# Kernel tuning notes

Measured on AMD Instinct MI355X. Metric: run time of the kernel, lower is better.

The kernel has to match this reference:

```python
import jax, jax.numpy as jnp
import numpy as np
from jax import lax

NEG = jnp.float32(-1e30)  # log-domain 'zero'
BLANK = 0


def setup_inputs() -> dict:
    T, N, C, S = 512, 512, 80, 128
    k0, k1, k2, k3 = jax.random.split(jax.random.key(0), 4)
    logits = jax.random.normal(k0, (T, N, C), dtype=jnp.float32)
    log_probs = jax.nn.log_softmax(logits, axis=-1)  # CTCLoss expects log-probs
    targets = jax.random.randint(k1, (N, S), 1, C).astype(jnp.int32)  # labels in [1, C-1], blank=0 excluded
    input_lengths = jax.random.randint(k2, (N,), T // 2, T + 1).astype(jnp.int32)
    target_lengths = jax.random.randint(k3, (N,), S // 2, S + 1).astype(jnp.int32)
    return {"log_probs": log_probs, "targets": targets,
            "input_lengths": input_lengths, "target_lengths": target_lengths}


def _ctc_loss(log_probs, targets, input_lengths, target_lengths):
    # log_probs: (T, N, C) log-probabilities; targets: (N, S) labels (no blanks)
    T, N, C = log_probs.shape
    S = targets.shape[1]
    L = 2 * S + 1  # extended label length: blank-interleaved

    # extended targets: [blank, y1, blank, y2, ..., yS, blank]  -> (N, L)
    ext = jnp.zeros((N, L), jnp.int32).at[:, 1::2].set(targets)
    # skip transition (s-2 -> s) allowed only if ext[s] != ext[s-2]
    # (blank positions have ext[s]==ext[s-2]==blank, so this also forbids blank skips)
    skip_ok = jnp.pad(ext[:, 2:] != ext[:, :-2], ((0, 0), (2, 0)), constant_values=False)

    # emission log-probs on the lattice: (T, N, L)
    emit = jnp.take_along_axis(log_probs, jnp.broadcast_to(ext[None], (T, N, L)), axis=2)

    # alpha at t=0: only lattice positions 0 (blank) and 1 (first label) reachable
    alpha0 = jnp.full((N, L), NEG).at[:, 0].set(emit[0, :, 0]).at[:, 1].set(emit[0, :, 1])

    def step(alpha, xs):
        em, t = xs  # em: (N, L)
        a1 = jnp.pad(alpha[:, :-1], ((0, 0), (1, 0)), constant_values=NEG)
        a2 = jnp.where(skip_ok,
                       jnp.pad(alpha[:, :-2], ((0, 0), (2, 0)), constant_values=NEG), NEG)
        m = jnp.maximum(alpha, jnp.maximum(a1, a2))
        lse = m + jnp.log(jnp.exp(alpha - m) + jnp.exp(a1 - m) + jnp.exp(a2 - m))
        new = lse + em
        # freeze alpha for finished sequences (t >= input_length)
        alpha_new = jnp.where((t < input_lengths)[:, None], new, alpha)
        return alpha_new, None

    alpha_T, _ = lax.scan(step, alpha0, (emit[1:], jnp.arange(1, T, dtype=jnp.int32)))

    # final states: last blank (2*tl) and last label (2*tl - 1)
    i1 = (2 * target_lengths)[:, None]
    v1 = jnp.take_along_axis(alpha_T, i1, axis=1)[:, 0]
    v2 = jnp.take_along_axis(alpha_T, i1 - 1, axis=1)[:, 0]
    m = jnp.maximum(v1, v2)
    loss = -(m + jnp.log(jnp.exp(v1 - m) + jnp.exp(v2 - m)))
    # zero_infinity=True: infeasible alignments -> 0 loss
    loss = jnp.where(jnp.isfinite(loss) & (loss < 1e10), loss, 0.0)
    return loss  # (N,) reduction='none'


def reference(log_probs, targets, input_lengths, target_lengths):
    return _ctc_loss(log_probs, targets, input_lengths, target_lengths)
```

## Files before the change

kernel.cpp:

```cpp
#include <hip/hip_runtime.h>


#define NEGC  (-1.0e30f)
#define LOG2E 1.4426950408889634f
#define LN2   0.6931471805599453f

constexpr int T_ = 512;
constexpr int C_ = 80;
constexpr int S_ = 128;
constexpr int U_ = 8;
constexpr int WROW = 520;

__device__ __forceinline__ float exp2a(float x) { return __builtin_amdgcn_exp2f(x); }
__device__ __forceinline__ float log2a(float x) { return __builtin_amdgcn_logf(x); }

template <int CTRL>
__device__ __forceinline__ float dppf(float old_, float src) {
    return __int_as_float(__builtin_amdgcn_update_dpp(
        __float_as_int(old_), __float_as_int(src), CTRL, 0xF, 0xF, false));
}

__device__ __forceinline__ float lse2(float x, float y) {
    float m = fmaxf(x, y);
    return m + log2a(1.0f + exp2a(-fabsf(x - y)));
}
__device__ __forceinline__ float lse3(float x, float y, float z) {
    float m = fmaxf(x, fmaxf(y, z));
    return m + log2a(exp2a(x - m) + exp2a(y - m) + exp2a(z - m));
}

__global__ __launch_bounds__(64) void ctc_half(
    const float* __restrict__ lp, const int* __restrict__ tgt,
    const int* __restrict__ ilen, const int* __restrict__ tlen,
    float* __restrict__ ws, int N)
{
    const int b   = blockIdx.x;
    const int n   = b >> 1;
    const int dir = b & 1;
    const int l   = threadIdx.x;

    float* ga = ws + (size_t)n * WROW;
    float* gg = ga + 260;

    const int* tn = tgt + n * S_;
    const int ext1 = tn[2 * l];
    const int ext3 = tn[2 * l + 1];
    const int prev = (l > 0) ? tn[2 * l - 1] : 0;
    const bool skip1 = (l > 0) && (ext1 != prev);
    const bool skip3 = (ext3 != ext1);
    const bool skb3  = (l < 63) && (tn[2 * l + 2] != ext3);

    int len = ilen[n];
    len = len < 1 ? 1 : (len > T_ ? T_ : len);
    const int mid = len >> 1;

    const size_t rstride = (size_t)N * C_;
    const float* lpn = lp + (size_t)n * C_;
    const float* pB = lpn;
    const float* p1 = lpn + ext1;
    const float* p3 = lpn + ext3;

    float rb[U_], r1[U_], r3[U_];

    if (dir == 0) {
        const int last = mid - 1 > 0 ? mid - 1 : 0;
        #pragma unroll
        for (int u = 0; u < U_; ++u) {
            const int r = u + 1;
            const int rc = r < mid ? r : last;
            const size_t o = (size_t)rc * rstride;
            rb[r & 7] = pB[o]; r1[r & 7] = p1[o]; r3[r & 7] = p3[o];
        }
        float a0 = NEGC, a1 = NEGC, a2 = NEGC, a3 = NEGC, a4 = NEGC;
        {
            const float i0 = pB[0] * LOG2E;
            const float i1 = p1[0] * LOG2E;
            if (l == 0) { a0 = i0; a1 = i1; }
        }
        for (int tb = 1; tb < mid; tb += U_) {
            #pragma unroll
            for (int u = 0; u < U_; ++u) {
                const int t = tb + u;
                const int slot = (1 + u) & 7;
                const float eb = rb[slot] * LOG2E;
                const float e1 = r1[slot] * LOG2E;
                const float e3 = r3[slot] * LOG2E;
                const int rr = t + U_;
                const int rc = rr < mid ? rr : last;
                const size_t o = (size_t)rc * rstride;
                const float nrb = pB[o], nr1 = p1[o], nr3 = p3[o];
                if (t < mid) {
                    const float sm1 = dppf<0x138>(NEGC, a3);
                    const float M = fmaxf(fmaxf(fmaxf(a0, a1), fmaxf(a2, a3)),
                                          fmaxf(a4, sm1));
                    const float q0 = exp2a(a0 - M);
                    const float q1 = exp2a(a1 - M);
                    const float q2 = exp2a(a2 - M);
                    const float q3 = exp2a(a3 - M);
                    const float q4 = exp2a(a4 - M);
                    const float qs = exp2a(sm1 - M);
                    const float Mb = M + eb;
                    a0 = log2a(q0 + qs)                      + Mb;
                    a1 = log2a(q1 + q0 + (skip1 ? qs : 0.f)) + M + e1;
                    a2 = log2a(q2 + q1)                      + Mb;
                    a3 = log2a(q3 + q2 + (skip3 ? q1 : 0.f)) + M + e3;
                    a4 = log2a(q4 + q3)                      + Mb;
                }
                rb[slot] = nrb; r1[slot] = nr1; r3[slot] = nr3;
            }
        }
        ga[4 * l + 0] = a0; ga[4 * l + 1] = a1;
        ga[4 * l + 2] = a2; ga[4 * l + 3] = a3;
        if (l == 63) ga[256] = a4;
    } else {
        const int fe = len - 1;
        #pragma unroll
        for (int u = 0; u < U_; ++u) {
            int rc = fe - 1 - u; if (rc < 0) rc = 0;
            const size_t o = (size_t)rc * rstride;
            rb[u] = pB[o]; r1[u] = p1[o]; r3[u] = p3[o];
        }
        const int tl = tlen[n];
        const int sA = 2 * tl, sB = 2 * tl - 1;
        float g0, g1, g2, g3, g4;
        {
            const size_t o = (size_t)fe * rstride;
            const float ebi = pB[o] * LOG2E;
            const float e1i = p1[o] * LOG2E;
            const float e3i = p3[o] * LOG2E;
            const int s0 = 4 * l;
            g0 = (s0     == sA)                 ? ebi : NEGC;
            g1 = (s0 + 1 == sA || s0 + 1 == sB) ? e1i : NEGC;
            g2 = (s0 + 2 == sA)                 ? ebi : NEGC;
            g3 = (s0 + 3 == sA || s0 + 3 == sB) ? e3i : NEGC;
            g4 = (l == 63 && 256 == sA)         ? ebi : NEGC;
        }
        for (int tb = fe - 1; tb >= mid; tb -= U_) {
            #pragma unroll
            for (int u = 0; u < U_; ++u) {
                const int t = tb - u;
                const int slot = ((fe - 1 - tb) + u) & 7;
                const float eb = rb[slot] * LOG2E;
                const float e1 = r1[slot] * LOG2E;
                const float e3 = r3[slot] * LOG2E;
                int rc = t - U_; if (rc < 0) rc = 0;
                const size_t o = (size_t)rc * rstride;
                const float nrb = pB[o], nr1 = p1[o], nr3 = p3[o];
                if (t >= mid) {
                    const float nx0 = dppf<0x130>(g4,   g0);
                    const float nx1 = dppf<0x130>(NEGC, g1);
                    const float M = fmaxf(fmaxf(fmaxf(g0, g1), fmaxf(g2, g3)),
                                          fmaxf(nx0, nx1));
                    const float q0 = exp2a(g0 - M);
                    const float q1 = exp2a(g1 - M);
                    const float q2 = exp2a(g2 - M);
                    const float q3 = exp2a(g3 - M);
                    const float qx0 = exp2a(nx0 - M);
                    const float qx1 = exp2a(nx1 - M);
                    const float skb1q = (ext3 != ext1) ? q3 : 0.f;
                    g0 = log2a(q0 + q1)                        + M + eb;
                    g1 = log2a(q1 + q2 + skb1q)                + M + e1;
                    g2 = log2a(q2 + q3)                        + M + eb;
                    g3 = log2a(q3 + qx0 + (skb3 ? qx1 : 0.f))  + M + e3;
                    g4 = g4 + eb;
                }
                rb[slot] = nrb; r1[slot] = nr1; r3[slot] = nr3;
            }
        }
        gg[4 * l + 0] = g0; gg[4 * l + 1] = g1;
        gg[4 * l + 2] = g2; gg[4 * l + 3] = g3;
        if (l == 63) gg[256] = g4;
    }
}

__global__ __launch_bounds__(64) void ctc_comb(
    const float* __restrict__ ws, const int* __restrict__ tgt,
    const int* __restrict__ ilen, const int* __restrict__ tlen,
    float* __restrict__ out, int N)
{
    const int n = blockIdx.x;
    const int l = threadIdx.x;
    const float* ga = ws + (size_t)n * WROW;
    const float* gg = ga + 260;

    int len = ilen[n];
    len = len < 1 ? 1 : (len > T_ ? T_ : len);
    const int tl = tlen[n];

    if (len == 1) {
        if (l == 0) {
            const float v1 = ga[2 * tl];
            const float v2 = (2 * tl >= 1) ? ga[2 * tl - 1] : NEGC;
            float loss = -lse2(v1, v2) * LN2;
            if (!(loss < 1e10f) || !isfinite(loss)) loss = 0.0f;
            out[n] = loss;
        }
        return;
    }

    const int* tn = tgt + n * S_;
    const int ext1 = tn[2 * l];
    const int ext3 = tn[2 * l + 1];
    const int prev = (l > 0) ? tn[2 * l - 1] : 0;
    const bool skip1 = (l > 0) && (ext1 != prev);
    const bool skip3 = (ext3 != ext1);

    const int s0 = 4 * l;
    const float Am1 = (l > 0) ? ga[s0 - 1] : NEGC;
    const float A0 = ga[s0], A1 = ga[s0 + 1], A2 = ga[s0 + 2], A3 = ga[s0 + 3];
    const float v0 = lse2(A0, Am1)                    + gg[s0];
    const float v1 = lse3(A1, A0, skip1 ? Am1 : NEGC) + gg[s0 + 1];
    const float v2 = lse2(A2, A1)                     + gg[s0 + 2];
    const float v3 = lse3(A3, A2, skip3 ? A1 : NEGC)  + gg[s0 + 3];
    const float v4 = (l == 63) ? (lse2(ga[256], A3) + gg[256]) : NEGC;

    float m = fmaxf(fmaxf(v0, v1), fmaxf(fmaxf(v2, v3), v4));
    float ssum = exp2a(v0 - m) + exp2a(v1 - m) + exp2a(v2 - m)
               + exp2a(v3 - m) + exp2a(v4 - m);
    float M = m;
    #pragma unroll
    for (int d = 1; d < 64; d <<= 1) M = fmaxf(M, __shfl_xor(M, d));
    float r = ssum * exp2a(m - M);
    #pragma unroll
    for (int d = 1; d < 64; d <<= 1) r += __shfl_xor(r, d);
    if (l == 0) {
        float loss = -LN2 * (M + log2a(r));
        if (!(loss < 1e10f) || !isfinite(loss)) loss = 0.0f;
        out[n] = loss;
    }
}

__global__ __launch_bounds__(128) void ctc_fused(
    const float* __restrict__ lp, const int* __restrict__ tgt,
    const int* __restrict__ ilen, const int* __restrict__ tlen,
    float* __restrict__ out, int N)
{
    const int n    = blockIdx.x;
    const int wave = threadIdx.x >> 6;
    const int l    = threadIdx.x & 63;

    __shared__ float ga[2 * S_ + 1];
    __shared__ float gg[2 * S_ + 1];

    const int* tn = tgt + n * S_;
    const int ext1 = tn[2 * l];
    const int ext3 = tn[2 * l + 1];
    const int prev = (l > 0) ? tn[2 * l - 1] : 0;
    const bool skip1 = (l > 0) && (ext1 != prev);
    const bool skip3 = (ext3 != ext1);
    const bool skb1 = (tn[2 * l + 1] != tn[2 * l]);
    const bool skb3 = (l < 63) && (tn[2 * l + 2] != tn[2 * l + 1]);

    int len = ilen[n];
    len = len < 1 ? 1 : (len > T_ ? T_ : len);
    const int mid = len >> 1;

    const size_t rstride = (size_t)N * C_;
    const float* lpn = lp + (size_t)n * C_;
    const float* pB = lpn;
    const float* p1 = lpn + ext1;
    const float* p3 = lpn + ext3;

    float rb[U_], r1[U_], r3[U_];

    if (wave == 0) {
        const int last = mid - 1 > 0 ? mid - 1 : 0;
        #pragma unroll
        for (int u = 0; u < U_; ++u) {
            const int r = u + 1;
            const int rc = r < mid ? r : last;
            const size_t o = (size_t)rc * rstride;
            rb[r & 7] = pB[o]; r1[r & 7] = p1[o]; r3[r & 7] = p3[o];
        }
        float a0 = NEGC, a1 = NEGC, a2 = NEGC, a3 = NEGC, a4 = NEGC;
        {
            const float i0 = pB[0] * LOG2E;
            const float i1 = p1[0] * LOG2E;
            if (l == 0) { a0 = i0; a1 = i1; }
        }
        for (int tb = 1; tb < mid; tb += U_) {
            #pragma unroll
            for (int u = 0; u < U_; ++u) {
                const int t = tb + u;
                const int slot = (1 + u) & 7;
                const float eb = rb[slot] * LOG2E;
                const float e1 = r1[slot] * LOG2E;
                const float e3 = r3[slot] * LOG2E;
                const int rr = t + U_;
                const int rc = rr < mid ? rr : last;
                const size_t o = (size_t)rc * rstride;
                const float nrb = pB[o], nr1 = p1[o], nr3 = p3[o];
                if (t < mid) {
                    const float sm1 = dppf<0x138>(NEGC, a3);
                    const float z1 = skip1 ? sm1 : NEGC;
                    const float z3 = skip3 ? a1  : NEGC;
                    const float n0 = lse2(a0, sm1)    + eb;
                    const float n1 = lse3(a1, a0, z1) + e1;
                    const float n2 = lse2(a2, a1)     + eb;
                    const float n3 = lse3(a3, a2, z3) + e3;
                    const float n4 = lse2(a4, a3)     + eb;
                    a0 = n0; a1 = n1; a2 = n2; a3 = n3; a4 = n4;
                }
                rb[slot] = nrb; r1[slot] = nr1; r3[slot] = nr3;
            }
        }
        ga[4 * l + 0] = a0; ga[4 * l + 1] = a1;
        ga[4 * l + 2] = a2; ga[4 * l + 3] = a3;
        if (l == 63) ga[256] = a4;
    } else {
        const int fe = len - 1;
        #pragma unroll
        for (int u = 0; u < U_; ++u) {
            int rc = fe - 1 - u; if (rc < 0) rc = 0;
            const size_t o = (size_t)rc * rstride;
            rb[u] = pB[o]; r1[u] = p1[o]; r3[u] = p3[o];
        }
        const int tl = tlen[n];
        const int sA = 2 * tl, sB = 2 * tl - 1;
        float g0, g1, g2, g3, g4;
        {
            const size_t o = (size_t)fe * rstride;
            const float ebi = pB[o] * LOG2E;
            const float e1i = p1[o] * LOG2E;
            const float e3i = p3[o] * LOG2E;
            const int s0 = 4 * l;
            g0 = (s0     == sA)                 ? ebi : NEGC;
            g1 = (s0 + 1 == sA || s0 + 1 == sB) ? e1i : NEGC;
            g2 = (s0 + 2 == sA)                 ? ebi : NEGC;
            g3 = (s0 + 3 == sA || s0 + 3 == sB) ? e3i : NEGC;
            g4 = (l == 63 && 256 == sA)         ? ebi : NEGC;
        }
        for (int tb = fe - 1; tb >= mid; tb -= U_) {
            #pragma unroll
            for (int u = 0; u < U_; ++u) {
                const int t = tb - u;
                const int slot = ((fe - 1 - tb) + u) & 7;
                const float eb = rb[slot] * LOG2E;
                const float e1 = r1[slot] * LOG2E;
                const float e3 = r3[slot] * LOG2E;
                int rc = t - U_; if (rc < 0) rc = 0;
                const size_t o = (size_t)rc * rstride;
                const float nrb = pB[o], nr1 = p1[o], nr3 = p3[o];
                if (t >= mid) {
                    const float nx0 = dppf<0x130>(g4,   g0);
                    const float nx1 = dppf<0x130>(NEGC, g1);
                    const float z1 = skb1 ? g3  : NEGC;
                    const float z3 = skb3 ? nx1 : NEGC;
                    const float n0 = lse2(g0, g1)      + eb;
                    const float n1 = lse3(g1, g2, z1)  + e1;
                    const float n2 = lse2(g2, g3)      + eb;
                    const float n3 = lse3(g3, nx0, z3) + e3;
                    const float n4 = g4 + eb;
                    g0 = n0; g1 = n1; g2 = n2; g3 = n3; g4 = n4;
                }
                rb[slot] = nrb; r1[slot] = nr1; r3[slot] = nr3;
            }
        }
        gg[4 * l + 0] = g0; gg[4 * l + 1] = g1;
        gg[4 * l + 2] = g2; gg[4 * l + 3] = g3;
        if (l == 63) gg[256] = g4;
    }

    __syncthreads();

    if (wave == 0) {
        const int tl = tlen[n];
        if (len == 1) {
            if (l == 0) {
                const float v1 = ga[2 * tl];
                const float v2 = (2 * tl >= 1) ? ga[2 * tl - 1] : NEGC;
                float loss = -lse2(v1, v2) * LN2;
                if (!(loss < 1e10f) || !isfinite(loss)) loss = 0.0f;
                out[n] = loss;
            }
            return;
        }
        const int s0 = 4 * l;
        const float Am1 = (l > 0) ? ga[s0 - 1] : NEGC;
        const float A0 = ga[s0], A1 = ga[s0 + 1], A2 = ga[s0 + 2], A3 = ga[s0 + 3];
        const float v0 = lse2(A0, Am1)                    + gg[s0];
        const float v1 = lse3(A1, A0, skip1 ? Am1 : NEGC) + gg[s0 + 1];
        const float v2 = lse2(A2, A1)                     + gg[s0 + 2];
        const float v3 = lse3(A3, A2, skip3 ? A1 : NEGC)  + gg[s0 + 3];
        const float v4 = (l == 63) ? (lse2(ga[256], A3) + gg[256]) : NEGC;

        float m = fmaxf(fmaxf(v0, v1), fmaxf(fmaxf(v2, v3), v4));
        float ssum = exp2a(v0 - m) + exp2a(v1 - m) + exp2a(v2 - m)
                   + exp2a(v3 - m) + exp2a(v4 - m);
        float M = m;
        #pragma unroll
        for (int d = 1; d < 64; d <<= 1) M = fmaxf(M, __shfl_xor(M, d));
        float r = ssum * exp2a(m - M);
        #pragma unroll
        for (int d = 1; d < 64; d <<= 1) r += __shfl_xor(r, d);
        if (l == 0) {
            float loss = -LN2 * (M + log2a(r));
            if (!(loss < 1e10f) || !isfinite(loss)) loss = 0.0f;
            out[n] = loss;
        }
    }
}

extern "C" void kernel_launch(void* const* d_in, const int* in_sizes, int n_in,
                              void* d_out, int out_size, void* d_ws, size_t ws_size,
                              hipStream_t stream) {
    const float* lp  = (const float*)d_in[0];
    const int*   tg  = (const int*)  d_in[1];
    const int*   il  = (const int*)  d_in[2];
    const int*   tl  = (const int*)  d_in[3];
    float*       out = (float*)d_out;
    const int N = in_sizes[2];
    const size_t need = (size_t)N * WROW * sizeof(float);
    if (ws_size >= need) {
        ctc_half<<<2 * N, 64, 0, stream>>>(lp, tg, il, tl, (float*)d_ws, N);
        ctc_comb<<<N, 64, 0, stream>>>((const float*)d_ws, tg, il, tl, out, N);
    } else {
        ctc_fused<<<N, 128, 0, stream>>>(lp, tg, il, tl, out, N);
    }
}
```

Baseline: 155.7 us.

## Run CTC recursion in linear probability domain with per-block wave rescaling

Both the forward and backward half-recursions now keep alpha/beta as scaled linear probabilities instead of log values. Each step becomes multiply-add with precomputed exp2 emissions, replacing six exp2 and five log2 calls per lane per step. Every 8 steps a DPP wave-wide max finds a shared exponent and the values are renormalised with ldexpf to avoid underflow. The trade-off is possible precision loss for states far below the wave max, which flush to zero, plus the extra reduction overhead per block.

```diff
diff --git a/kernel.cpp b/kernel.cpp
--- a/kernel.cpp
+++ b/kernel.cpp
@@ -18,6 +18,16 @@
 __device__ __forceinline__ float dppf(float old_, float src) {
     return __int_as_float(__builtin_amdgcn_update_dpp(
         __float_as_int(old_), __float_as_int(src), CTRL, 0xF, 0xF, false));
+}
+
+__device__ __forceinline__ int wave_max_bits(float m) {
+    m = fmaxf(m, dppf<0x111>(m, m));
+    m = fmaxf(m, dppf<0x112>(m, m));
+    m = fmaxf(m, dppf<0x114>(m, m));
+    m = fmaxf(m, dppf<0x118>(m, m));
+    m = fmaxf(m, dppf<0x142>(m, m));
+    m = fmaxf(m, dppf<0x143>(m, m));
+    return __builtin_amdgcn_readlane(__float_as_int(m), 63);
 }
 
 __device__ __forceinline__ float lse2(float x, float y) {
@@ -71,47 +81,54 @@
             const size_t o = (size_t)rc * rstride;
             rb[r & 7] = pB[o]; r1[r & 7] = p1[o]; r3[r & 7] = p3[o];
         }
-        float a0 = NEGC, a1 = NEGC, a2 = NEGC, a3 = NEGC, a4 = NEGC;
-        {
-            const float i0 = pB[0] * LOG2E;
-            const float i1 = p1[0] * LOG2E;
-            if (l == 0) { a0 = i0; a1 = i1; }
-        }
+        float p0_ = 0.f, p1_ = 0.f, p2_ = 0.f, p3_ = 0.f, p4_ = 0.f;
+        int   E = -60;
+        if (l == 0) {
+            p0_ = exp2a(pB[0] * LOG2E + 60.0f);
+            p1_ = exp2a(p1[0] * LOG2E + 60.0f);
+        }
+        float PbC = exp2a(rb[1] * LOG2E);
+        float P1C = exp2a(r1[1] * LOG2E);
+        float P3C = exp2a(r3[1] * LOG2E);
         for (int tb = 1; tb < mid; tb += U_) {
             #pragma unroll
             for (int u = 0; u < U_; ++u) {
                 const int t = tb + u;
                 const int slot = (1 + u) & 7;
-                const float eb = rb[slot] * LOG2E;
-                const float e1 = r1[slot] * LOG2E;
-                const float e3 = r3[slot] * LOG2E;
                 const int rr = t + U_;
                 const int rc = rr < mid ? rr : last;
                 const size_t o = (size_t)rc * rstride;
                 const float nrb = pB[o], nr1 = p1[o], nr3 = p3[o];
+                const int ns = (2 + u) & 7;
+                const float PbN = exp2a(rb[ns] * LOG2E);
+                const float P1N = exp2a(r1[ns] * LOG2E);
+                const float P3N = exp2a(r3[ns] * LOG2E);
                 if (t < mid) {
-                    const float sm1 = dppf<0x138>(NEGC, a3);
-                    const float M = fmaxf(fmaxf(fmaxf(a0, a1), fmaxf(a2, a3)),
-                                          fmaxf(a4, sm1));
-                    const float q0 = exp2a(a0 - M);
-                    const float q1 = exp2a(a1 - M);
-                    const float q2 = exp2a(a2 - M);
-                    const float q3 = exp2a(a3 - M);
-                    const float q4 = exp2a(a4 - M);
-                    const float qs = exp2a(sm1 - M);
-                    const float Mb = M + eb;
-                    a0 = log2a(q0 + qs)                      + Mb;
-                    a1 = log2a(q1 + q0 + (skip1 ? qs : 0.f)) + M + e1;
-                    a2 = log2a(q2 + q1)                      + Mb;
-                    a3 = log2a(q3 + q2 + (skip3 ? q1 : 0.f)) + M + e3;
-                    a4 = log2a(q4 + q3)                      + Mb;
+                    const float sm1 = dppf<0x138>(0.0f, p3_);
+                    const float i0 = p0_ + sm1;
+                    const float i1 = p1_ + p0_ + (skip1 ? sm1 : 0.f);
+                    const float i2 = p2_ + p1_;
+                    const float i3 = p3_ + p2_ + (skip3 ? p1_ : 0.f);
+                    const float i4 = p4_ + p3_;
+                    p0_ = i0 * PbC; p1_ = i1 * P1C; p2_ = i2 * PbC;
+                    p3_ = i3 * P3C; p4_ = i4 * PbC;
                 }
+                PbC = PbN; P1C = P1N; P3C = P3N;
                 rb[slot] = nrb; r1[slot] = nr1; r3[slot] = nr3;
             }
-        }
-        ga[4 * l + 0] = a0; ga[4 * l + 1] = a1;
-        ga[4 * l + 2] = a2; ga[4 * l + 3] = a3;
-        if (l == 63) ga[256] = a4;
+            const int mi = wave_max_bits(
+                fmaxf(fmaxf(fmaxf(p0_, p1_), fmaxf(p2_, p3_)), p4_));
+            const int e = (mi > 0) ? (((mi >> 23) & 255) - 187) : 0;
+            E += e;
+            p0_ = ldexpf(p0_, -e); p1_ = ldexpf(p1_, -e); p2_ = ldexpf(p2_, -e);
+            p3_ = ldexpf(p3_, -e); p4_ = ldexpf(p4_, -e);
+        }
+        const float fE = (float)E;
+        ga[4 * l + 0] = (p0_ > 0.f) ? fmaxf(log2a(p0_) + fE, NEGC) : NEGC;
+        ga[4 * l + 1] = (p1_ > 0.f) ? fmaxf(log2a(p1_) + fE, NEGC) : NEGC;
+        ga[4 * l + 2] = (p2_ > 0.f) ? fmaxf(log2a(p2_) + fE, NEGC) : NEGC;
+        ga[4 * l + 3] = (p3_ > 0.f) ? fmaxf(log2a(p3_) + fE, NEGC) : NEGC;
+        if (l == 63) ga[256] = (p4_ > 0.f) ? fmaxf(log2a(p4_) + fE, NEGC) : NEGC;
     } else {
         const int fe = len - 1;
         #pragma unroll
@@ -122,54 +139,61 @@
         }
         const int tl = tlen[n];
         const int sA = 2 * tl, sB = 2 * tl - 1;
-        float g0, g1, g2, g3, g4;
+        float g0_, g1_, g2_, g3_, g4_;
+        int E = -60;
         {
             const size_t o = (size_t)fe * rstride;
-            const float ebi = pB[o] * LOG2E;
-            const float e1i = p1[o] * LOG2E;
-            const float e3i = p3[o] * LOG2E;
+            const float ebi = pB[o] * LOG2E + 60.0f;
+            const float e1i = p1[o] * LOG2E + 60.0f;
+            const float e3i = p3[o] * LOG2E + 60.0f;
             const int s0 = 4 * l;
-            g0 = (s0     == sA)                 ? ebi : NEGC;
-            g1 = (s0 + 1 == sA || s0 + 1 == sB) ? e1i : NEGC;
-            g2 = (s0 + 2 == sA)                 ? ebi : NEGC;
-            g3 = (s0 + 3 == sA || s0 + 3 == sB) ? e3i : NEGC;
-            g4 = (l == 63 && 256 == sA)         ? ebi : NEGC;
-        }
+            g0_ = (s0     == sA)                 ? exp2a(ebi) : 0.f;
+            g1_ = (s0 + 1 == sA || s0 + 1 == sB) ? exp2a(e1i) : 0.f;
+            g2_ = (s0 + 2 == sA)                 ? exp2a(ebi) : 0.f;
+            g3_ = (s0 + 3 == sA || s0 + 3 == sB) ? exp2a(e3i) : 0.f;
+            g4_ = (l == 63 && 256 == sA)         ? exp2a(ebi) : 0.f;
+        }
+        float PbC = exp2a(rb[0] * LOG2E);
+        float P1C = exp2a(r1[0] * LOG2E);
+        float P3C = exp2a(r3[0] * LOG2E);
         for (int tb = fe - 1; tb >= mid; tb -= U_) {
             #pragma unroll
             for (int u = 0; u < U_; ++u) {
                 const int t = tb - u;
-                const int slot = ((fe - 1 - tb) + u) & 7;
-                const float eb = rb[slot] * LOG2E;
-                const float e1 = r1[slot] * LOG2E;
-                const float e3 = r3[slot] * LOG2E;
+                const int slot = u;
                 int rc = t - U_; if (rc < 0) rc = 0;
                 const size_t o = (size_t)rc * rstride;
                 const float nrb = pB[o], nr1 = p1[o], nr3 = p3[o];
+                const int ns = (u + 1) & 7;
+                const float PbN = exp2a(rb[ns] * LOG2E);
+                const float P1N = exp2a(r1[ns] * LOG2E);
+                const float P3N = exp2a(r3[ns] * LOG2E);
                 if (t >= mid) {
-                    const float nx0 = dppf<0x130>(g4,   g0);
-                    const float nx1 = dppf<0x130>(NEGC, g1);
-                    const float M = fmaxf(fmaxf(fmaxf(g0, g1), fmaxf(g2, g3)),
-                                          fmaxf(nx0, nx1));
-                    const float q0 = exp2a(g0 - M);
-                    const float q1 = exp2a(g1 - M);
-                    const float q2 = exp2a(g2 - M);
-                    const float q3 = exp2a(g3 - M);
-                    const float qx0 = exp2a(nx0 - M);
-                    const float qx1 = exp2a(nx1 - M);
-                    const float skb1q = (ext3 != ext1) ? q3 : 0.f;
-                    g0 = log2a(q0 + q1)                        + M + eb;
-                    g1 = log2a(q1 + q2 + skb1q)                + M + e1;
-                    g2 = log2a(q2 + q3)                        + M + eb;
-                    g3 = log2a(q3 + qx0 + (skb3 ? qx1 : 0.f))  + M + e3;
-                    g4 = g4 + eb;
+                    const float x0 = dppf<0x130>(g4_, g0_);
+                    const float x1 = dppf<0x130>(0.f, g1_);
+                    const float i0 = g0_ + g1_;
+                    const float i1 = g1_ + g2_ + (skip3 ? g3_ : 0.f);
+                    const float i2 = g2_ + g3_;
+                    const float i3 = g3_ + x0 + (skb3 ? x1 : 0.f);
+                    g0_ = i0 * PbC; g1_ = i1 * P1C; g2_ = i2 * PbC;
+                    g3_ = i3 * P3C; g4_ = g4_ * PbC;
                 }
+                PbC = PbN; P1C = P1N; P3C = P3N;
                 rb[slot] = nrb; r1[slot] = nr1; r3[slot] = nr3;
             }
-        }
-        gg[4 * l + 0] = g0; gg[4 * l + 1] = g1;
-        gg[4 * l + 2] = g2; gg[4 * l + 3] = g3;
-        if (l == 63) gg[256] = g4;
+            const int mi = wave_max_bits(
+                fmaxf(fmaxf(fmaxf(g0_, g1_), fmaxf(g2_, g3_)), g4_));
+            const int e = (mi > 0) ? (((mi >> 23) & 255) - 187) : 0;
+            E += e;
+            g0_ = ldexpf(g0_, -e); g1_ = ldexpf(g1_, -e); g2_ = ldexpf(g2_, -e);
+            g3_ = ldexpf(g3_, -e); g4_ = ldexpf(g4_, -e);
+        }
+        const float fE = (float)E;
+        gg[4 * l + 0] = (g0_ > 0.f) ? fmaxf(log2a(g0_) + fE, NEGC) : NEGC;
+        gg[4 * l + 1] = (g1_ > 0.f) ? fmaxf(log2a(g1_) + fE, NEGC) : NEGC;
+        gg[4 * l + 2] = (g2_ > 0.f) ? fmaxf(log2a(g2_) + fE, NEGC) : NEGC;
+        gg[4 * l + 3] = (g3_ > 0.f) ? fmaxf(log2a(g3_) + fE, NEGC) : NEGC;
+        if (l == 63) gg[256] = (g4_ > 0.f) ? fmaxf(log2a(g4_) + fE, NEGC) : NEGC;
     }
 }
 
```

Measured after the change: 148.8 us. -4.4%, faster.
